# Kernel optimization log

Hardware: AMD Instinct MI355X
Metric: run time of the kernel (lower is better)

## Reference

```python
import jax, jax.numpy as jnp
import numpy as np


def gcn_conv(x, W, b, src, dst, n_nodes):
    # PyG GCNConv: out = D^{-1/2} (A+I) D^{-1/2} X W + b  (self-loops already in src/dst)
    h = x @ W  # [N, F_out]
    ones = jnp.ones(src.shape[0], dtype=h.dtype)
    deg = jax.ops.segment_sum(ones, dst, num_segments=n_nodes)  # in-degree incl. self-loop
    dinv = jnp.where(deg > 0, jax.lax.rsqrt(deg), 0.0)
    norm = dinv[src] * dinv[dst]  # [E]
    msg = h[src] * norm[:, None]  # gather + scale, [E, F_out]
    out = jax.ops.segment_sum(msg, dst, num_segments=n_nodes)  # scatter-add
    return out + b


def setup_inputs() -> dict:
    key = jax.random.key(0)
    ks = jax.random.split(key, 5)
    N, E, F_in, H, F_out = 50000, 800000, 128, 128, 64
    x = jax.random.normal(ks[0], (N, F_in), dtype=jnp.float32)
    edge_index = jax.random.randint(ks[1], (2, E), 0, N, dtype=jnp.int64)
    W1 = jax.random.normal(ks[2], (F_in, H), dtype=jnp.float32) / np.sqrt(F_in)
    b1 = jnp.zeros((H,), dtype=jnp.float32)
    W3 = jax.random.normal(ks[3], (H, F_out), dtype=jnp.float32) / np.sqrt(H)
    b3 = jnp.zeros((F_out,), dtype=jnp.float32)
    W4 = jax.random.normal(ks[4], (H, F_out), dtype=jnp.float32) / np.sqrt(H)
    b4 = jnp.zeros((F_out,), dtype=jnp.float32)
    return {"x": x, "edge_index": edge_index, "W1": W1, "b1": b1,
            "W3": W3, "b3": b3, "W4": W4, "b4": b4}


def reference(x, edge_index, W1, b1, W3, b3, W4, b4):
    n_nodes = x.shape[0]
    loops = jnp.arange(n_nodes, dtype=edge_index.dtype)
    src = jnp.concatenate([edge_index[0], loops])
    dst = jnp.concatenate([edge_index[1], loops])
    h = jax.nn.relu(gcn_conv(x, W1, b1, src, dst, n_nodes))  # dropout p=0.0 is identity
    mean = gcn_conv(h, W3, b3, src, dst, n_nodes)
    std = gcn_conv(h, W4, b4, src, dst, n_nodes)
    return (mean, std)
```

## Files before the change

### kernel.cpp

```cpp
#include <hip/hip_runtime.h>

typedef unsigned int uint_t;
typedef unsigned short ushort_t;

constexpr int MAXDEG = 64;

static __device__ __forceinline__ uint_t f2bf_bits(float f) {
  uint_t u = __builtin_bit_cast(uint_t, f);
  return (u + 0x7fffu + ((u >> 16) & 1u)) >> 16;
}
static __device__ __forceinline__ uint_t pack_bf2(float lo, float hi) {
  return f2bf_bits(lo) | (f2bf_bits(hi) << 16);
}
static __device__ __forceinline__ float bf_lo(uint_t u) {
  return __builtin_bit_cast(float, u << 16);
}
static __device__ __forceinline__ float bf_hi(uint_t u) {
  return __builtin_bit_cast(float, u & 0xffff0000u);
}

typedef __attribute__((ext_vector_type(2))) uint_t v2u;
typedef __attribute__((ext_vector_type(8))) short  short8_t;
typedef __attribute__((ext_vector_type(4))) float  f32x4_t;

static __device__ __forceinline__ void stnt_u2(uint_t* p, uint_t a, uint_t b) {
  v2u t; t.x = a; t.y = b;
  __builtin_nontemporal_store(t, (v2u*)p);
}

static inline size_t align256(size_t x) { return (x + 255) & ~(size_t)255; }

__global__ __launch_bounds__(256) void bucket_scatter_kernel(
    const int* __restrict__ src, const int* __restrict__ dst,
    uint2* __restrict__ buckets, int* __restrict__ bucketcnt,
    int E, int C, int shift, int NB) {
  __shared__ int hist[512];
  __shared__ int base[512];
  const int tid = threadIdx.x;
  const int e0 = blockIdx.x * 2048;

  for (int i = tid; i < NB; i += 256) hist[i] = 0;
  __syncthreads();

  int dd[8], ss[8], slot[8];
#pragma unroll
  for (int i = 0; i < 8; ++i) {
    int e = e0 + tid + i * 256;
    bool ok = (e < E);
    dd[i] = ok ? dst[e] : -1;
    ss[i] = ok ? src[e] : 0;
    slot[i] = ok ? atomicAdd(&hist[dd[i] >> shift], 1) : 0;
  }
  __syncthreads();

  for (int i = tid; i < NB; i += 256) {
    int c = hist[i];
    base[i] = (c > 0) ? atomicAdd(&bucketcnt[i], c) : 0;
  }
  __syncthreads();

#pragma unroll
  for (int i = 0; i < 8; ++i) {
    if (dd[i] < 0) continue;
    int b = dd[i] >> shift;
    int pos = base[b] + slot[i];
    if (pos < C)
      buckets[(size_t)b * C + pos] = make_uint2((uint_t)dd[i], (uint_t)ss[i]);
  }
}

template<typename IdxT, int WIN>
__global__ __launch_bounds__(256) void bucket_to_rows_kernel(
    const uint2* __restrict__ buckets, const int* __restrict__ bucketcnt,
    IdxT* __restrict__ edge, int* __restrict__ deg, int Nn, int C, int shift) {
  __shared__ __align__(16) IdxT rows[WIN * MAXDEG];
  __shared__ int cnt[WIN];
  const int tid = threadIdx.x;
  const int b = blockIdx.x;
  const int node0 = b << shift;
  const int RANGE = 1 << shift;
  int ec = bucketcnt[b];
  if (ec > C) ec = C;
  const uint2* bb = buckets + (size_t)b * C;

  for (int w0 = 0; w0 < RANGE; w0 += WIN) {
    for (int i = tid; i < WIN; i += 256) cnt[i] = 0;
    __syncthreads();
    for (int i = tid; i < ec; i += 256) {
      uint2 it = bb[i];
      int local = (int)it.x - node0 - w0;
      if (local >= 0 && local < WIN) {
        int sl = atomicAdd(&cnt[local], 1);
        if (sl < MAXDEG) rows[local * MAXDEG + sl] = (IdxT)it.y;
      }
    }
    __syncthreads();
    const int nbase = node0 + w0;
    constexpr int PER = (MAXDEG * sizeof(IdxT)) / 16;
    const uint4* rv = (const uint4*)rows;
    uint4* ev = (uint4*)(edge + (size_t)nbase * MAXDEG);
    for (int i = tid; i < WIN * PER; i += 256) {
      int node = nbase + i / PER;
      if (node < Nn) ev[i] = rv[i];
    }
    for (int i = tid; i < WIN; i += 256) {
      int node = nbase + i;
      if (node < Nn) deg[node] = cnt[i];
    }
    __syncthreads();
  }
}

__global__ __launch_bounds__(256) void gemm1_kernel(
    const float* __restrict__ X, const float* __restrict__ W1,
    uint_t* __restrict__ outG, int Nrows) {
  constexpr int BK = 64;
  __shared__ float wlds[BK][128];
  __shared__ float xT[BK][68];

  const int tid = threadIdx.x;
  const int cg = tid & 31;
  const int rl = tid >> 5;
  const int rowbase = blockIdx.x * 64;

  float acc[8][4];
#pragma unroll
  for (int i = 0; i < 8; ++i)
#pragma unroll
    for (int j = 0; j < 4; ++j) acc[i][j] = 0.f;

  for (int k0 = 0; k0 < 128; k0 += BK) {
    __syncthreads();
#pragma unroll
    for (int i = 0; i < 8; ++i) {
      int f = tid + i * 256;
      int kk = f >> 5, cc = f & 31;
      float4 v = ((const float4*)W1)[(size_t)(k0 + kk) * 32 + cc];
      *(float4*)&wlds[kk][cc * 4] = v;
    }
    {
      int r = tid >> 2;
      int rg = rowbase + r;
      int rs = (rg < Nrows) ? rg : (Nrows - 1);
      const float4* xrow = (const float4*)(X + (size_t)rs * 128);
      bool valid = (rg < Nrows);
#pragma unroll
      for (int p = 0; p < 4; ++p) {
        int kf4 = (tid & 3) + p * 4;
        float4 v = xrow[(k0 >> 2) + kf4];
        if (!valid) v = make_float4(0.f, 0.f, 0.f, 0.f);
        int ke = kf4 * 4;
        xT[ke + 0][r] = v.x;
        xT[ke + 1][r] = v.y;
        xT[ke + 2][r] = v.z;
        xT[ke + 3][r] = v.w;
      }
    }
    __syncthreads();
#pragma unroll 8
    for (int kk = 0; kk < BK; ++kk) {
      float4 xa = *(const float4*)&xT[kk][rl * 8];
      float4 xb = *(const float4*)&xT[kk][rl * 8 + 4];
      float4 wv = *(const float4*)&wlds[kk][cg * 4];
      float xr[8] = {xa.x, xa.y, xa.z, xa.w, xb.x, xb.y, xb.z, xb.w};
      float wc[4] = {wv.x, wv.y, wv.z, wv.w};
#pragma unroll
      for (int i = 0; i < 8; ++i)
#pragma unroll
        for (int j = 0; j < 4; ++j)
          acc[i][j] = fmaf(xr[i], wc[j], acc[i][j]);
    }
  }
#pragma unroll
  for (int i = 0; i < 8; ++i) {
    int r = rowbase + rl * 8 + i;
    if (r >= Nrows) continue;
    stnt_u2(outG + (size_t)r * 64 + cg * 2,
            pack_bf2(acc[i][0], acc[i][1]), pack_bf2(acc[i][2], acc[i][3]));
  }
}

__global__ __launch_bounds__(256) void pack_w_kernel(
    const float* __restrict__ W3, const float* __restrict__ W4,
    ushort_t* __restrict__ Bhi, ushort_t* __restrict__ Blo) {
  int u = blockIdx.x * 256 + threadIdx.x;
  int l = u & 63, kk = (u >> 6) & 3, t = u >> 8;
  int q = l >> 4, c = l & 15;
  int n = t * 16 + c;
  short8_t vh, vl;
#pragma unroll
  for (int j = 0; j < 8; ++j) {
    int k = kk * 32 + q * 8 + j;
    float w = (n < 64) ? W3[(size_t)k * 64 + n] : W4[(size_t)k * 64 + (n - 64)];
    uint_t hb = f2bf_bits(w);
    float wl = w - __builtin_bit_cast(float, hb << 16);
    vh[j] = (short)hb;
    vl[j] = (short)f2bf_bits(wl);
  }
  *(short8_t*)(Bhi + (size_t)u * 8) = vh;
  *(short8_t*)(Blo + (size_t)u * 8) = vl;
}

__global__ __launch_bounds__(256) void gemm2_mfma_kernel(
    const ushort_t* __restrict__ Xbf, const ushort_t* __restrict__ Bhi,
    const ushort_t* __restrict__ Blo, const float* __restrict__ b3,
    const float* __restrict__ b4, float* __restrict__ outM,
    float* __restrict__ outS, int Nrows) {
  const int tid = threadIdx.x;
  const int wid = tid >> 6;
  const int lane = tid & 63;
  const int q = lane >> 4;
  const int c = lane & 15;
  const int rowbase = blockIdx.x * 64 + wid * 16;

  f32x4_t acc[8];
#pragma unroll
  for (int t = 0; t < 8; ++t) acc[t] = (f32x4_t){0.f, 0.f, 0.f, 0.f};

  int arow = rowbase + c;
  int ars = (arow < Nrows) ? arow : (Nrows - 1);
  const ushort_t* abase = Xbf + (size_t)ars * 128 + q * 8;

#pragma unroll
  for (int kk = 0; kk < 4; ++kk) {
    short8_t a = __builtin_nontemporal_load((const short8_t*)(abase + kk * 32));
#pragma unroll
    for (int t = 0; t < 8; ++t) {
      const size_t fo = ((size_t)(t * 4 + kk) * 64 + lane) * 8;
      short8_t bh = *(const short8_t*)(Bhi + fo);
      short8_t bl = *(const short8_t*)(Blo + fo);
      acc[t] = __builtin_amdgcn_mfma_f32_16x16x32_bf16(a, bh, acc[t], 0, 0, 0);
      acc[t] = __builtin_amdgcn_mfma_f32_16x16x32_bf16(a, bl, acc[t], 0, 0, 0);
    }
  }

#pragma unroll
  for (int t = 0; t < 8; ++t) {
    float bias = (t < 4) ? b3[t * 16 + c] : b4[(t - 4) * 16 + c];
    float* obase = (t < 4) ? (outM + t * 16 + c) : (outS + (t - 4) * 16 + c);
#pragma unroll
    for (int rr = 0; rr < 4; ++rr) {
      int row = rowbase + q * 4 + rr;
      if (row < Nrows)
        __builtin_nontemporal_store(acc[t][rr] + bias, obase + (size_t)row * 64);
    }
  }
}

template<int EPI, bool SRCDV, typename IdxT>
__global__ __launch_bounds__(256) void aggregate_kernel(
    const uint_t* __restrict__ g, const int* __restrict__ deg,
    const IdxT* __restrict__ edge, const float* __restrict__ b1,
    uint_t* __restrict__ out, int Nn) {
  const int wave = threadIdx.x >> 6;
  const int lane = threadIdx.x & 63;
  const int n = blockIdx.x * 4 + wave;
  if (n >= Nn) return;
  const int dn = deg[n];
  const int cnt = (dn > 63) ? 63 : dn;
  const float sc = rsqrtf((float)(dn + 1));

  int vl = n;
  if (lane >= 1 && lane <= cnt) vl = (int)edge[(size_t)n * MAXDEG + (lane - 1)];
  float wl = 0.f;
  if (lane == 0)        wl = SRCDV ? sc : 1.f;
  else if (lane <= cnt) wl = SRCDV ? rsqrtf((float)(deg[vl] + 1)) : 1.f;

  const int h = lane >> 5;
  const int c = lane & 31;
  const uint_t* gc = g + c * 2;

  float a0 = 0.f, a1 = 0.f, a2 = 0.f, a3 = 0.f;
  const int entries = cnt + 1;
  const int npairs = (entries + 1) >> 1;

  int p = 0;
  for (; p + 4 <= npairs; p += 4) {
    int ss[4]; float ww[4]; uint2 uu[4];
#pragma unroll
    for (int t = 0; t < 4; ++t) {
      int j = 2 * (p + t) + h;
      ss[t] = __shfl(vl, j);
      ww[t] = __shfl(wl, j);
    }
#pragma unroll
    for (int t = 0; t < 4; ++t)
      uu[t] = *(const uint2*)(gc + (size_t)ss[t] * 64);
#pragma unroll
    for (int t = 0; t < 4; ++t) {
      a0 = fmaf(ww[t], bf_lo(uu[t].x), a0);
      a1 = fmaf(ww[t], bf_hi(uu[t].x), a1);
      a2 = fmaf(ww[t], bf_lo(uu[t].y), a2);
      a3 = fmaf(ww[t], bf_hi(uu[t].y), a3);
    }
  }
  for (; p < npairs; ++p) {
    int j = 2 * p + h;
    int s0 = __shfl(vl, j);
    float w0 = __shfl(wl, j);
    uint2 u = *(const uint2*)(gc + (size_t)s0 * 64);
    a0 = fmaf(w0, bf_lo(u.x), a0);
    a1 = fmaf(w0, bf_hi(u.x), a1);
    a2 = fmaf(w0, bf_lo(u.y), a2);
    a3 = fmaf(w0, bf_hi(u.y), a3);
  }

  a0 += __shfl_xor(a0, 32);
  a1 += __shfl_xor(a1, 32);
  a2 += __shfl_xor(a2, 32);
  a3 += __shfl_xor(a3, 32);

  if (h == 0) {
    if (EPI == 1) {
      float4 b = ((const float4*)b1)[c];
      a0 = fmaxf(fmaf(sc, a0, b.x), 0.f) * sc;
      a1 = fmaxf(fmaf(sc, a1, b.y), 0.f) * sc;
      a2 = fmaxf(fmaf(sc, a2, b.z), 0.f) * sc;
      a3 = fmaxf(fmaf(sc, a3, b.w), 0.f) * sc;
    } else {
      a0 *= sc; a1 *= sc; a2 *= sc; a3 *= sc;
    }
    stnt_u2(out + (size_t)n * 64 + c * 2, pack_bf2(a0, a1), pack_bf2(a2, a3));
  }
}

extern "C" void kernel_launch(void* const* d_in, const int* in_sizes, int n_in,
                              void* d_out, int out_size, void* d_ws, size_t ws_size,
                              hipStream_t stream) {
  const float* x  = (const float*)d_in[0];
  const int*   ei = (const int*)d_in[1];
  const float* W1 = (const float*)d_in[2];
  const float* b1 = (const float*)d_in[3];
  const float* W3 = (const float*)d_in[4];
  const float* b3 = (const float*)d_in[5];
  const float* W4 = (const float*)d_in[6];
  const float* b4 = (const float*)d_in[7];

  const int N = in_sizes[0] / 128;
  const int E = in_sizes[1] / 2;
  const int* src = ei;
  const int* dst = ei + E;
  const bool small = (N <= 65535);
  const size_t esz = small ? sizeof(ushort_t) : sizeof(int);

  int shift = 7;
  while (((N + (1 << shift) - 1) >> shift) > 512) ++shift;
  const int NB = (N + (1 << shift) - 1) >> shift;
  const int C = (E / NB) * 3 / 2 + 512;

  char* w = (char*)d_ws;
  size_t off = 0;
  auto carve = [&](size_t bytes) { void* p = w + off; off = align256(off + bytes); return p; };
  int*      deg       = (int*)carve((size_t)N * sizeof(int));
  int*      bucketcnt = (int*)carve(512 * sizeof(int));
  uint2*    buckets   = (uint2*)carve((size_t)NB * C * sizeof(uint2));
  void*     edge      = carve((size_t)N * MAXDEG * esz);
  uint_t*   bufG      = (uint_t*)carve((size_t)N * 64 * sizeof(uint_t));
  uint_t*   bufH      = (uint_t*)carve((size_t)N * 64 * sizeof(uint_t));
  ushort_t* Bhi       = (ushort_t*)carve((size_t)16384 * sizeof(ushort_t));
  ushort_t* Blo       = (ushort_t*)carve((size_t)16384 * sizeof(ushort_t));

  float* out_mean = (float*)d_out;
  float* out_std  = out_mean + (size_t)N * 64;

  hipMemsetAsync(bucketcnt, 0, 512 * sizeof(int), stream);

  const int gblocks = (N + 63) / 64;
  const int ablocks = (N + 3) / 4;
  const int sblocks = (E + 2047) / 2048;

  pack_w_kernel<<<8, 256, 0, stream>>>(W3, W4, Bhi, Blo);
  bucket_scatter_kernel<<<sblocks, 256, 0, stream>>>(src, dst, buckets, bucketcnt, E, C, shift, NB);

  if (small) {
    ushort_t* es = (ushort_t*)edge;
    bucket_to_rows_kernel<ushort_t, 128><<<NB, 256, 0, stream>>>(
        buckets, bucketcnt, es, deg, N, C, shift);
    gemm1_kernel<<<gblocks, 256, 0, stream>>>(x, W1, bufG, N);
    aggregate_kernel<1, true,  ushort_t><<<ablocks, 256, 0, stream>>>(bufG, deg, es, b1, bufH, N);
    aggregate_kernel<2, false, ushort_t><<<ablocks, 256, 0, stream>>>(bufH, deg, es, nullptr, bufG, N);
  } else {
    int* es = (int*)edge;
    bucket_to_rows_kernel<int, 128><<<NB, 256, 0, stream>>>(
        buckets, bucketcnt, es, deg, N, C, shift);
    gemm1_kernel<<<gblocks, 256, 0, stream>>>(x, W1, bufG, N);
    aggregate_kernel<1, true,  int><<<ablocks, 256, 0, stream>>>(bufG, deg, es, b1, bufH, N);
    aggregate_kernel<2, false, int><<<ablocks, 256, 0, stream>>>(bufH, deg, es, nullptr, bufG, N);
  }
  gemm2_mfma_kernel<<<gblocks, 256, 0, stream>>>(
      (const ushort_t*)bufG, Bhi, Blo, b3, b4, out_mean, out_std, N);
}
```

Baseline: 145.6 us.

## Replace scalar FP32 first-layer GEMM with split-bf16 MFMA and fold memset into pack kernel

The first-layer X@W1 GEMM moves from a scalar FMA kernel using LDS tiles to a bf16 MFMA kernel that emulates fp32 with a three-term hi/lo split (hi*hi, hi*lo, lo*hi). W1 is pre-packed into MFMA fragment layout by the extended pack kernel. That kernel now also zeroes the bucket counters, which removes the separate memset call. The aim is to cut GEMM compute time and one launch, at the cost of extra MFMA work for the split and scattered 2-byte output stores. Bounds clamps are also added in the bucket code.

```diff
diff --git a/kernel.cpp b/kernel.cpp
--- a/kernel.cpp
+++ b/kernel.cpp
@@ -64,7 +64,7 @@
     if (dd[i] < 0) continue;
     int b = dd[i] >> shift;
     int pos = base[b] + slot[i];
-    if (pos < C)
+    if (pos >= 0 && pos < C)
       buckets[(size_t)b * C + pos] = make_uint2((uint_t)dd[i], (uint_t)ss[i]);
   }
 }
@@ -81,6 +81,7 @@
   const int RANGE = 1 << shift;
   int ec = bucketcnt[b];
   if (ec > C) ec = C;
+  if (ec < 0) ec = 0;
   const uint2* bb = buckets + (size_t)b * C;
 
   for (int w0 = 0; w0 < RANGE; w0 += WIN) {
@@ -111,79 +112,18 @@
   }
 }
 
-__global__ __launch_bounds__(256) void gemm1_kernel(
-    const float* __restrict__ X, const float* __restrict__ W1,
-    uint_t* __restrict__ outG, int Nrows) {
-  constexpr int BK = 64;
-  __shared__ float wlds[BK][128];
-  __shared__ float xT[BK][68];
-
-  const int tid = threadIdx.x;
-  const int cg = tid & 31;
-  const int rl = tid >> 5;
-  const int rowbase = blockIdx.x * 64;
-
-  float acc[8][4];
-#pragma unroll
-  for (int i = 0; i < 8; ++i)
-#pragma unroll
-    for (int j = 0; j < 4; ++j) acc[i][j] = 0.f;
-
-  for (int k0 = 0; k0 < 128; k0 += BK) {
-    __syncthreads();
-#pragma unroll
-    for (int i = 0; i < 8; ++i) {
-      int f = tid + i * 256;
-      int kk = f >> 5, cc = f & 31;
-      float4 v = ((const float4*)W1)[(size_t)(k0 + kk) * 32 + cc];
-      *(float4*)&wlds[kk][cc * 4] = v;
-    }
-    {
-      int r = tid >> 2;
-      int rg = rowbase + r;
-      int rs = (rg < Nrows) ? rg : (Nrows - 1);
-      const float4* xrow = (const float4*)(X + (size_t)rs * 128);
-      bool valid = (rg < Nrows);
-#pragma unroll
-      for (int p = 0; p < 4; ++p) {
-        int kf4 = (tid & 3) + p * 4;
-        float4 v = xrow[(k0 >> 2) + kf4];
-        if (!valid) v = make_float4(0.f, 0.f, 0.f, 0.f);
-        int ke = kf4 * 4;
-        xT[ke + 0][r] = v.x;
-        xT[ke + 1][r] = v.y;
-        xT[ke + 2][r] = v.z;
-        xT[ke + 3][r] = v.w;
-      }
-    }
-    __syncthreads();
-#pragma unroll 8
-    for (int kk = 0; kk < BK; ++kk) {
-      float4 xa = *(const float4*)&xT[kk][rl * 8];
-      float4 xb = *(const float4*)&xT[kk][rl * 8 + 4];
-      float4 wv = *(const float4*)&wlds[kk][cg * 4];
-      float xr[8] = {xa.x, xa.y, xa.z, xa.w, xb.x, xb.y, xb.z, xb.w};
-      float wc[4] = {wv.x, wv.y, wv.z, wv.w};
-#pragma unroll
-      for (int i = 0; i < 8; ++i)
-#pragma unroll
-        for (int j = 0; j < 4; ++j)
-          acc[i][j] = fmaf(xr[i], wc[j], acc[i][j]);
-    }
-  }
-#pragma unroll
-  for (int i = 0; i < 8; ++i) {
-    int r = rowbase + rl * 8 + i;
-    if (r >= Nrows) continue;
-    stnt_u2(outG + (size_t)r * 64 + cg * 2,
-            pack_bf2(acc[i][0], acc[i][1]), pack_bf2(acc[i][2], acc[i][3]));
-  }
-}
-
 __global__ __launch_bounds__(256) void pack_w_kernel(
-    const float* __restrict__ W3, const float* __restrict__ W4,
-    ushort_t* __restrict__ Bhi, ushort_t* __restrict__ Blo) {
-  int u = blockIdx.x * 256 + threadIdx.x;
+    const float* __restrict__ W1, const float* __restrict__ W3,
+    const float* __restrict__ W4,
+    ushort_t* __restrict__ B1hi, ushort_t* __restrict__ B1lo,
+    ushort_t* __restrict__ B2hi, ushort_t* __restrict__ B2lo,
+    int* __restrict__ bucketcnt) {
+  if (blockIdx.x == 0) {
+    bucketcnt[threadIdx.x] = 0;
+    bucketcnt[threadIdx.x + 256] = 0;
+  }
+  const bool w1 = (blockIdx.x < 8);
+  int u = (w1 ? blockIdx.x : blockIdx.x - 8) * 256 + threadIdx.x;
   int l = u & 63, kk = (u >> 6) & 3, t = u >> 8;
   int q = l >> 4, c = l & 15;
   int n = t * 16 + c;
@@ -191,14 +131,73 @@
 #pragma unroll
   for (int j = 0; j < 8; ++j) {
     int k = kk * 32 + q * 8 + j;
-    float w = (n < 64) ? W3[(size_t)k * 64 + n] : W4[(size_t)k * 64 + (n - 64)];
+    float w;
+    if (w1)          w = W1[(size_t)k * 128 + n];
+    else if (n < 64) w = W3[(size_t)k * 64 + n];
+    else             w = W4[(size_t)k * 64 + (n - 64)];
     uint_t hb = f2bf_bits(w);
     float wl = w - __builtin_bit_cast(float, hb << 16);
     vh[j] = (short)hb;
     vl[j] = (short)f2bf_bits(wl);
   }
-  *(short8_t*)(Bhi + (size_t)u * 8) = vh;
-  *(short8_t*)(Blo + (size_t)u * 8) = vl;
+  ushort_t* ph = w1 ? B1hi : B2hi;
+  ushort_t* pl = w1 ? B1lo : B2lo;
+  *(short8_t*)(ph + (size_t)u * 8) = vh;
+  *(short8_t*)(pl + (size_t)u * 8) = vl;
+}
+
+__global__ __launch_bounds__(256) void gemm1_mfma_kernel(
+    const float* __restrict__ X, const ushort_t* __restrict__ Bhi,
+    const ushort_t* __restrict__ Blo, ushort_t* __restrict__ outG, int Nrows) {
+  const int tid = threadIdx.x;
+  const int wid = tid >> 6;
+  const int lane = tid & 63;
+  const int q = lane >> 4;
+  const int c = lane & 15;
+  const int rowbase = blockIdx.x * 64 + wid * 16;
+
+  f32x4_t acc[8];
+#pragma unroll
+  for (int t = 0; t < 8; ++t) acc[t] = (f32x4_t){0.f, 0.f, 0.f, 0.f};
+
+  int arow = rowbase + c;
+  int ars = (arow < Nrows) ? arow : (Nrows - 1);
+  const float* abase = X + (size_t)ars * 128 + q * 8;
+
+#pragma unroll
+  for (int kk = 0; kk < 4; ++kk) {
+    float4 xa = *(const float4*)(abase + kk * 32);
+    float4 xb = *(const float4*)(abase + kk * 32 + 4);
+    float xf[8] = {xa.x, xa.y, xa.z, xa.w, xb.x, xb.y, xb.z, xb.w};
+    short8_t ahi, alo;
+#pragma unroll
+    for (int j = 0; j < 8; ++j) {
+      float f = xf[j];
+      uint_t hb = f2bf_bits(f);
+      ahi[j] = (short)hb;
+      float fl = f - __builtin_bit_cast(float, hb << 16);
+      alo[j] = (short)f2bf_bits(fl);
+    }
+#pragma unroll
+    for (int t = 0; t < 8; ++t) {
+      const size_t fo = ((size_t)(t * 4 + kk) * 64 + lane) * 8;
+      short8_t bh = *(const short8_t*)(Bhi + fo);
+      short8_t bl = *(const short8_t*)(Blo + fo);
+      acc[t] = __builtin_amdgcn_mfma_f32_16x16x32_bf16(ahi, bh, acc[t], 0, 0, 0);
+      acc[t] = __builtin_amdgcn_mfma_f32_16x16x32_bf16(ahi, bl, acc[t], 0, 0, 0);
+      acc[t] = __builtin_amdgcn_mfma_f32_16x16x32_bf16(alo, bh, acc[t], 0, 0, 0);
+    }
+  }
+
+#pragma unroll
+  for (int t = 0; t < 8; ++t) {
+#pragma unroll
+    for (int rr = 0; rr < 4; ++rr) {
+      int row = rowbase + q * 4 + rr;
+      if (row < Nrows)
+        outG[(size_t)row * 128 + t * 16 + c] = (ushort_t)f2bf_bits(acc[t][rr]);
+    }
+  }
 }
 
 __global__ __launch_bounds__(256) void gemm2_mfma_kernel(
@@ -357,36 +356,36 @@
   void*     edge      = carve((size_t)N * MAXDEG * esz);
   uint_t*   bufG      = (uint_t*)carve((size_t)N * 64 * sizeof(uint_t));
   uint_t*   bufH      = (uint_t*)carve((size_t)N * 64 * sizeof(uint_t));
-  ushort_t* Bhi       = (ushort_t*)carve((size_t)16384 * sizeof(ushort_t));
-  ushort_t* Blo       = (ushort_t*)carve((size_t)16384 * sizeof(ushort_t));
+  ushort_t* B1hi      = (ushort_t*)carve((size_t)16384 * sizeof(ushort_t));
+  ushort_t* B1lo      = (ushort_t*)carve((size_t)16384 * sizeof(ushort_t));
+  ushort_t* B2hi      = (ushort_t*)carve((size_t)16384 * sizeof(ushort_t));
+  ushort_t* B2lo      = (ushort_t*)carve((size_t)16384 * sizeof(ushort_t));
 
   float* out_mean = (float*)d_out;
   float* out_std  = out_mean + (size_t)N * 64;
-
-  hipMemsetAsync(bucketcnt, 0, 512 * sizeof(int), stream);
 
   const int gblocks = (N + 63) / 64;
   const int ablocks = (N + 3) / 4;
   const int sblocks = (E + 2047) / 2048;
 
-  pack_w_kernel<<<8, 256, 0, stream>>>(W3, W4, Bhi, Blo);
+  pack_w_kernel<<<16, 256, 0, stream>>>(W1, W3, W4, B1hi, B1lo, B2hi, B2lo, bucketcnt);
   bucket_scatter_kernel<<<sblocks, 256, 0, stream>>>(src, dst, buckets, bucketcnt, E, C, shift, NB);
 
   if (small) {
     ushort_t* es = (ushort_t*)edge;
     bucket_to_rows_kernel<ushort_t, 128><<<NB, 256, 0, stream>>>(
         buckets, bucketcnt, es, deg, N, C, shift);
-    gemm1_kernel<<<gblocks, 256, 0, stream>>>(x, W1, bufG, N);
+    gemm1_mfma_kernel<<<gblocks, 256, 0, stream>>>(x, B1hi, B1lo, (ushort_t*)bufG, N);
     aggregate_kernel<1, true,  ushort_t><<<ablocks, 256, 0, stream>>>(bufG, deg, es, b1, bufH, N);
     aggregate_kernel<2, false, ushort_t><<<ablocks, 256, 0, stream>>>(bufH, deg, es, nullptr, bufG, N);
   } else {
     int* es = (int*)edge;
     bucket_to_rows_kernel<int, 128><<<NB, 256, 0, stream>>>(
         buckets, bucketcnt, es, deg, N, C, shift);
-    gemm1_kernel<<<gblocks, 256, 0, stream>>>(x, W1, bufG, N);
+    gemm1_mfma_kernel<<<gblocks, 256, 0, stream>>>(x, B1hi, B1lo, (ushort_t*)bufG, N);
     aggregate_kernel<1, true,  int><<<ablocks, 256, 0, stream>>>(bufG, deg, es, b1, bufH, N);
     aggregate_kernel<2, false, int><<<ablocks, 256, 0, stream>>>(bufH, deg, es, nullptr, bufG, N);
   }
   gemm2_mfma_kernel<<<gblocks, 256, 0, stream>>>(
-      (const ushort_t*)bufG, Bhi, Blo, b3, b4, out_mean, out_std, N);
-}
+      (const ushort_t*)bufG, B2hi, B2lo, b3, b4, out_mean, out_std, N);
+}
```

Measured after the change: 126.2 us. 13.3% less time.
